# Kernel optimization log

Measured on AMD Instinct MI355X. Metric: run time of the kernel, lower is better.

The kernel has to match this reference:

```python
import jax, jax.numpy as jnp
import numpy as np

N_AE = 64
N_GRAPHS = 4096
N_ELE = 16384
EPS = 1e-5


def _seg_mean(v, idx, num_segments):
    s = jax.ops.segment_sum(v, idx, num_segments=num_segments)
    c = jax.ops.segment_sum(jnp.ones((v.shape[0], 1), v.dtype), idx, num_segments=num_segments)
    return s / jnp.maximum(c, 1.0)


def _batchnorm(h, gamma, beta):
    mu = jnp.mean(h, axis=0)
    var = jnp.mean(jnp.square(h - mu), axis=0)  # biased, as torch BN training fwd
    return (h - mu) * jax.lax.rsqrt(var + EPS) * gamma + beta


def _dist_layer(x, dist_feat, atom_idx, ele_idx, W, b, gamma, beta):
    # x: [N, 2*n_ae]
    pa = jax.nn.relu(_seg_mean(x[:, :N_AE], atom_idx, N_GRAPHS))[atom_idx]   # [N, n_ae]
    pe = jax.nn.relu(_seg_mean(x[:, N_AE:], ele_idx, N_ELE))[ele_idx]        # [N, n_ae]
    h = jnp.concatenate([dist_feat, pa, pe], axis=1)                          # [N, n_de+2*n_ae]
    h = h @ W.T + b                                                           # [N, 2*n_ae]
    h = _batchnorm(h, gamma, beta)
    return jax.nn.relu(h + x)


def setup_inputs() -> dict:
    key = jax.random.key(0)
    ks = jax.random.split(key, 12)
    N = 500000
    n_re = 64
    n_be = 64
    d = 2 * N_AE
    inp = {
        "x": jax.random.normal(ks[0], (N, d), jnp.float32),
        "rdf_feat": jax.random.normal(ks[1], (N, n_re), jnp.float32),
        "bdf_feat": jax.random.normal(ks[2], (N, n_be), jnp.float32),
        "atom_idx": jnp.sort(jax.random.randint(ks[3], (N,), 0, N_GRAPHS)),
        "ele_idx": jax.random.randint(ks[4], (N,), 0, N_ELE),
        "rdf_W": jax.random.normal(ks[5], (d, n_re + d), jnp.float32) * 0.05,
        "rdf_b": jnp.zeros((d,), jnp.float32),
        "rdf_gamma": jnp.ones((d,), jnp.float32),
        "rdf_beta": jnp.zeros((d,), jnp.float32),
        "bdf_W": jax.random.normal(ks[6], (d, n_be + d), jnp.float32) * 0.05,
        "bdf_b": jnp.zeros((d,), jnp.float32),
        "bdf_gamma": jnp.ones((d,), jnp.float32),
        "bdf_beta": jnp.zeros((d,), jnp.float32),
        "fc_W": jax.random.normal(ks[7], (d, 2 * d), jnp.float32) * 0.05,
        "fc_b": jnp.zeros((d,), jnp.float32),
    }
    return inp


def reference(x, rdf_feat, bdf_feat, atom_idx, ele_idx,
              rdf_W, rdf_b, rdf_gamma, rdf_beta,
              bdf_W, bdf_b, bdf_gamma, bdf_beta,
              fc_W, fc_b):
    x1 = _dist_layer(x, rdf_feat, atom_idx, ele_idx, rdf_W, rdf_b, rdf_gamma, rdf_beta)
    x2 = _dist_layer(x, bdf_feat, atom_idx, ele_idx, bdf_W, bdf_b, bdf_gamma, bdf_beta)
    h = jnp.concatenate([x1, x2], axis=1)  # [N, 4*n_ae]
    return jax.nn.relu(h @ fc_W.T + fc_b)  # [N, 2*n_ae]
```

## Files before the change

kernel.cpp:

```cpp
#include <hip/hip_runtime.h>
#include <hip/hip_bf16.h>

#define N_GRAPHS 4096
#define N_ELE 16384
#define EPS 1e-5f

#define A_TAB_OFF 0
#define A_CNT_OFF 262144
#define E_TAB_OFF 266240
#define E_CNT_OFF 1314816
#define STAT_OFF  1331200
#define ZPAD_OFF  1347584
#define ZERO_WORDS 1347588
#define A_TABH_OFF 1347600
#define E_TABH_OFF 1478672
#define W1PK_OFF  2002960
#define FCPK_OFF  2027536
#define SCALE_OFF 2043920
#define SHIFT_OFF 2044176
#define WS_WORDS  2044432

typedef __attribute__((ext_vector_type(8))) short bf16x8;
typedef __attribute__((ext_vector_type(4))) float f32x4;

__device__ __forceinline__ float bf2f(unsigned s) { return __uint_as_float(s << 16); }
__device__ __forceinline__ unsigned f2bf(float f) {
  unsigned u = __float_as_uint(f);
  return (u + 0x7fffu + ((u >> 16) & 1u)) >> 16;
}
__device__ __forceinline__ unsigned pkbf(float a, float b) {
  union { __hip_bfloat16 h; unsigned short u; } ca, cb;
  ca.h = __float2bfloat16(a); cb.h = __float2bfloat16(b);
  return (unsigned)ca.u | ((unsigned)cb.u << 16);
}
__device__ __forceinline__ void gload16(const void* g, void* l) {
  __builtin_amdgcn_global_load_lds(
      (const __attribute__((address_space(1))) unsigned*)g,
      (__attribute__((address_space(3))) unsigned*)l, 16, 0, 0);
}


__global__ void k_prep(const float* __restrict__ W1, const float* __restrict__ W2,
                       const float* __restrict__ fcW, float* __restrict__ ws) {
  int tid = blockIdx.x * 512 + threadIdx.x;
  if (tid < 49152) {
    unsigned short* wpk = (unsigned short*)(ws + W1PK_OFF);
    int L = tid / 24576, rem = tid % 24576;
    int ct = rem / 3072, rem2 = rem % 3072;
    int i = rem2 >> 9, lane = (rem2 >> 3) & 63, j = rem2 & 7;
    int zkb = L ? (i + 2) : (i < 2 ? i : i + 2);
    int zk = zkb * 32 + ((lane >> 4) << 3) + j;
    int kp = L ? (zk - 64) : (zk < 64 ? zk : zk - 64);
    int col = ct * 16 + (lane & 15);
    const float* W = L ? W2 : W1;
    wpk[tid] = (unsigned short)f2bf(W[col * 192 + kp]);
  } else {
    int idx = tid - 49152;
    unsigned short* fpk = (unsigned short*)(ws + FCPK_OFF);
    int ct = idx >> 12, kb = (idx >> 9) & 7, lane = (idx >> 3) & 63, j = idx & 7;
    fpk[idx] = (unsigned short)f2bf(fcW[(ct * 16 + (lane & 15)) * 256 + kb * 32 + ((lane >> 4) << 3) + j]);
  }
}

__global__ void k_seg(const float* __restrict__ x, const int* __restrict__ aidx,
                      const int* __restrict__ eidx, float* __restrict__ ws, int N) {
  float* A_tab = ws + A_TAB_OFF; float* A_cnt = ws + A_CNT_OFF;
  float* E_tab = ws + E_TAB_OFF; float* E_cnt = ws + E_CNT_OFF;
  int t = threadIdx.x;
  int c = t & 63, p = (t >> 6) & 1, s = t >> 7;
  int r0 = blockIdx.x * 256;
  int rend = min(r0 + 256, N);
  if (p == 0) {
    float acc = 0.f, cnt = 0.f; int cur = -1;
    for (int r = r0 + s; r < rend; r += 2) {
      int a = aidx[r];
      float v = x[(size_t)r * 128 + c];
      if (a != cur) {
        if (cur >= 0) { atomicAdd(&A_tab[cur * 64 + c], acc); if (c == 0) atomicAdd(&A_cnt[cur], cnt); }
        cur = a; acc = v; cnt = 1.f;
      } else { acc += v; cnt += 1.f; }
    }
    if (cur >= 0) { atomicAdd(&A_tab[cur * 64 + c], acc); if (c == 0) atomicAdd(&A_cnt[cur], cnt); }
  } else {
    for (int r = r0 + s; r < rend; r += 2) {
      int e = eidx[r];
      float v = x[(size_t)r * 128 + 64 + c];
      atomicAdd(&E_tab[e * 64 + c], v);
      if (c == 0) atomicAdd(&E_cnt[e], 1.f);
    }
  }
}

__global__ void k_fin(float* __restrict__ ws) {
  int i = blockIdx.x * 256 + threadIdx.x;
  unsigned* w32 = (unsigned*)ws;
  if (i < 131072) {
    int e = 2 * i;
    float cnt = fmaxf(ws[A_CNT_OFF + (e >> 6)], 1.f);
    float v0 = fmaxf(ws[A_TAB_OFF + e] / cnt, 0.f);
    float v1 = fmaxf(ws[A_TAB_OFF + e + 1] / cnt, 0.f);
    w32[A_TABH_OFF + i] = f2bf(v0) | (f2bf(v1) << 16);
  }
  if (i < 524288) {
    int e = 2 * i;
    float cnt = fmaxf(ws[E_CNT_OFF + (e >> 6)], 1.f);
    float v0 = fmaxf(ws[E_TAB_OFF + e] / cnt, 0.f);
    float v1 = fmaxf(ws[E_TAB_OFF + e + 1] / cnt, 0.f);
    w32[E_TABH_OFF + i] = f2bf(v0) | (f2bf(v1) << 16);
  }
}

__global__ __launch_bounds__(512) void k_gemm(
    const float* __restrict__ rdf, const float* __restrict__ bdf,
    const int* __restrict__ aidx, const int* __restrict__ eidx,
    float* __restrict__ ws, unsigned* __restrict__ outp, int N) {
  __shared__ __align__(16) char smem[32768];
  const unsigned short* Atabh = (const unsigned short*)(ws + A_TABH_OFF);
  const unsigned short* Etabh = (const unsigned short*)(ws + E_TABH_OFF);
  const void* zpad = (const void*)(ws + ZPAD_OFF);
  int t = threadIdx.x;
  int l = t & 63, w = t >> 6;
  int row0 = blockIdx.x * 64;

  #pragma unroll
  for (int ii = 0; ii < 2; ++ii) {
    int rb = (w * 2 + ii) * 4;
    int r = rb + (l >> 4);
    int srow = row0 + r;
    bool ok = srow < N;
    int s = l & 15;
    int c = (s & 8) | ((s ^ r) & 7);
    const void* src;
    if (c < 8) {
      int ia = ok ? aidx[srow] : 0;
      src = (const void*)(Atabh + ((size_t)ia * 64 + c * 8));
    } else {
      int ie = ok ? eidx[srow] : 0;
      src = (const void*)(Etabh + ((size_t)ie * 64 + (c - 8) * 8));
    }
    if (!ok) src = zpad;
    gload16(src, smem + 16384 + rb * 256);
  }

  {
    int r = t >> 3, c0 = (t & 7) * 2;
    int row = row0 + r;
    bool ok = row < N;
    #pragma unroll
    for (int cc = 0; cc < 2; ++cc) {
      int c = c0 + cc;
      uint4 wv;
      if (ok) {
        const float4* src = (const float4*)(c < 8 ? rdf + (size_t)row * 64 + c * 8
                                                  : bdf + (size_t)row * 64 + (c - 8) * 8);
        float4 f0 = src[0], f1 = src[1];
        wv.x = pkbf(f0.x, f0.y); wv.y = pkbf(f0.z, f0.w);
        wv.z = pkbf(f1.x, f1.y); wv.w = pkbf(f1.z, f1.w);
      } else wv = (uint4){0u, 0u, 0u, 0u};
      int slot = (c & 8) | ((c ^ r) & 7);
      *(uint4*)(smem + r * 256 + slot * 16) = wv;
    }
  }
  __syncthreads();

  int L = w >> 2, ctp = w & 3;
  const unsigned short* WpkL = (const unsigned short*)(ws + W1PK_OFF) + L * 24576;
  f32x4 acc[4][2];
  #pragma unroll
  for (int mt = 0; mt < 4; ++mt)
    #pragma unroll
    for (int cti = 0; cti < 2; ++cti) acc[mt][cti] = (f32x4){0.f, 0.f, 0.f, 0.f};
  int half = l >> 4;
  #pragma unroll
  for (int i = 0; i < 6; ++i) {
    int zkb = L ? (i + 2) : (i < 2 ? i : i + 2);
    int cg = zkb * 4 + half;
    const char* base = smem + (zkb < 4 ? 0 : 16384);
    int cl = cg & 15;
    bf16x8 af[4];
    #pragma unroll
    for (int mt = 0; mt < 4; ++mt) {
      int rr = mt * 16 + (l & 15);
      int slot = (cl & 8) | ((cl ^ rr) & 7);
      af[mt] = *(const bf16x8*)(base + rr * 256 + slot * 16);
    }
    #pragma unroll
    for (int cti = 0; cti < 2; ++cti) {
      bf16x8 bfr = *(const bf16x8*)(WpkL + (((ctp * 2 + cti) * 6 + i) * 64 + l) * 8);
      #pragma unroll
      for (int mt = 0; mt < 4; ++mt)
        acc[mt][cti] = __builtin_amdgcn_mfma_f32_16x16x32_bf16(af[mt], bfr, acc[mt][cti], 0, 0, 0);
    }
  }

  float* stat = ws + STAT_OFF + (blockIdx.x & 31) * 512;
  #pragma unroll
  for (int cti = 0; cti < 2; ++cti) {
    float s = 0.f, q = 0.f;
    #pragma unroll
    for (int mt = 0; mt < 4; ++mt)
      #pragma unroll
      for (int rr = 0; rr < 4; ++rr) { float v = acc[mt][cti][rr]; s += v; q += v * v; }
    s += __shfl_xor(s, 16); s += __shfl_xor(s, 32);
    q += __shfl_xor(q, 16); q += __shfl_xor(q, 32);
    if (l < 16) {
      int gc = L * 128 + ctp * 32 + cti * 16 + l;
      atomicAdd(&stat[gc], s);
      atomicAdd(&stat[256 + gc], q);
    }
  }
  __syncthreads();

  #pragma unroll
  for (int mt = 0; mt < 4; ++mt)
    #pragma unroll
    for (int cti = 0; cti < 2; ++cti)
      #pragma unroll
      for (int rr = 0; rr < 4; ++rr) {
        unsigned ub = pkbf(acc[mt][cti][rr], 0.f) & 0xffffu;
        unsigned pb = (unsigned)__shfl_xor((int)ub, 1);
        if (!(l & 1)) {
          int orow = mt * 16 + ((l >> 4) << 2) + rr;
          int colp = (L * 128 + ctp * 32 + cti * 16 + (l & 15)) >> 1;
          int c = colp >> 2;
          int ec = ((c ^ orow) & 7) | (c & 24);
          *(unsigned*)(smem + orow * 512 + ec * 16 + (colp & 3) * 4) = ub | (pb << 16);
        }
      }
  __syncthreads();
  #pragma unroll
  for (int p = 0; p < 4; ++p) {
    int e = p * 512 + t; int rr = e >> 5, v4 = e & 31;
    int ec = ((v4 ^ rr) & 7) | (v4 & 24);
    uint4 val = *(const uint4*)(smem + rr * 512 + ec * 16);
    if (row0 + rr < N) ((uint4*)outp)[(size_t)(row0 + rr) * 32 + v4] = val;
  }
}

__global__ void k_bnfin(const float* __restrict__ g1, const float* __restrict__ b1,
                        const float* __restrict__ g2, const float* __restrict__ b2,
                        float* __restrict__ ws, int N) {
  int c = threadIdx.x;
  float s = 0.f, q = 0.f;
  for (int m = 0; m < 32; ++m) { s += ws[STAT_OFF + m * 512 + c]; q += ws[STAT_OFF + m * 512 + 256 + c]; }
  float inv = 1.f / (float)N;
  float mu = s * inv;
  float var = fmaxf(q * inv - mu * mu, 0.f);
  int lyr = c >> 7, cc = c & 127;
  float ga = lyr ? g2[cc] : g1[cc];
  float be = lyr ? b2[cc] : b1[cc];
  float sc = ga * rsqrtf(var + EPS);
  ws[SCALE_OFF + c] = sc;
  ws[SHIFT_OFF + c] = be - mu * sc;
}

__global__ __launch_bounds__(512) void k_fc(
    const float* __restrict__ x, const float* __restrict__ fcb,
    float* __restrict__ ws, float* __restrict__ out, int N) {
  __shared__ __align__(16) char smem[32768];
  __shared__ float scsh[512];
  int t = threadIdx.x;
  int l = t & 63, w = t >> 6;
  int r = t >> 3, g = t & 7;
  const unsigned* hp = (const unsigned*)out;
  int row0 = blockIdx.x * 64;
  int row = row0 + r;
  bool ok = row < N;
  uint4 hv[4]; float4 xv[8];
  if (ok) {
    const uint4* hs = (const uint4*)(hp + (size_t)row * 128 + g * 16);
    #pragma unroll
    for (int i = 0; i < 4; ++i) hv[i] = hs[i];
    const float4* xs = (const float4*)(x + (size_t)row * 128 + (g & 3) * 32);
    #pragma unroll
    for (int i = 0; i < 8; ++i) xv[i] = xs[i];
  } else {
    #pragma unroll
    for (int i = 0; i < 4; ++i) hv[i] = (uint4){0u, 0u, 0u, 0u};
    #pragma unroll
    for (int i = 0; i < 8; ++i) xv[i] = (float4){0.f, 0.f, 0.f, 0.f};
  }
  scsh[t] = ws[SCALE_OFF + t];
  __syncthreads();
  {
    unsigned wv[16];
    const unsigned* hu = (const unsigned*)hv;
    const float* xf = (const float*)xv;
    #pragma unroll
    for (int j = 0; j < 16; ++j) {
      int c = g * 32 + 2 * j;
      float lo = bf2f(hu[j] & 0xffffu) * scsh[c]     + scsh[256 + c]     + xf[2 * j];
      float hi = bf2f(hu[j] >> 16)     * scsh[c + 1] + scsh[256 + c + 1] + xf[2 * j + 1];
      wv[j] = pkbf(fmaxf(lo, 0.f), fmaxf(hi, 0.f));
    }
    #pragma unroll
    for (int i = 0; i < 4; ++i) {
      int slot = ((g ^ r ^ i) & 7) | (i << 3);
      *(uint4*)(smem + r * 512 + slot * 16) = ((uint4*)wv)[i];
    }
  }
  __syncthreads();
  f32x4 acc[4];
  #pragma unroll
  for (int mt = 0; mt < 4; ++mt) acc[mt] = (f32x4){0.f, 0.f, 0.f, 0.f};
  const unsigned short* Fpk = (const unsigned short*)(ws + FCPK_OFF);
  int half = l >> 4;
  #pragma unroll
  for (int kb = 0; kb < 8; ++kb) {
    bf16x8 bfr = *(const bf16x8*)(Fpk + ((w * 8 + kb) * 64 + l) * 8);
    #pragma unroll
    for (int mt = 0; mt < 4; ++mt) {
      int rr = mt * 16 + (l & 15);
      int slot = ((kb ^ rr ^ half) & 7) | (half << 3);
      bf16x8 af = *(const bf16x8*)(smem + rr * 512 + slot * 16);
      acc[mt] = __builtin_amdgcn_mfma_f32_16x16x32_bf16(af, bfr, acc[mt], 0, 0, 0);
    }
  }
  float bias = fcb[(w << 4) + (l & 15)];
  __syncthreads();
  #pragma unroll
  for (int mt = 0; mt < 4; ++mt)
    #pragma unroll
    for (int rr = 0; rr < 4; ++rr) {
      int orow = mt * 16 + ((l >> 4) << 2) + rr;
      int col = (w << 4) + (l & 15);
      int c = col >> 2;
      int ec = ((c ^ orow) & 7) | (c & 24);
      *(float*)(smem + orow * 512 + ec * 16 + (col & 3) * 4) = fmaxf(acc[mt][rr] + bias, 0.f);
    }
  __syncthreads();
  #pragma unroll
  for (int p = 0; p < 4; ++p) {
    int e = p * 512 + t; int rr = e >> 5, v4 = e & 31;
    int ec = ((v4 ^ rr) & 7) | (v4 & 24);
    float4 val = *(const float4*)(smem + rr * 512 + ec * 16);
    if (row0 + rr < N) ((float4*)out)[(size_t)(row0 + rr) * 32 + v4] = val;
  }
}

extern "C" void kernel_launch(void* const* d_in, const int* in_sizes, int n_in,
                              void* d_out, int out_size, void* d_ws, size_t ws_size,
                              hipStream_t stream) {
  const float* x    = (const float*)d_in[0];
  const float* rdf  = (const float*)d_in[1];
  const float* bdf  = (const float*)d_in[2];
  const int*   aidx = (const int*)d_in[3];
  const int*   eidx = (const int*)d_in[4];
  const float* rdfW = (const float*)d_in[5];
  const float* rdfG = (const float*)d_in[7];
  const float* rdfBe= (const float*)d_in[8];
  const float* bdfW = (const float*)d_in[9];
  const float* bdfG = (const float*)d_in[11];
  const float* bdfBe= (const float*)d_in[12];
  const float* fcW  = (const float*)d_in[13];
  const float* fcB  = (const float*)d_in[14];
  float* out = (float*)d_out;
  float* ws  = (float*)d_ws;
  int N = in_sizes[0] / 128;
  int nT = (N + 63) / 64;

  hipMemsetAsync(d_ws, 0, (size_t)ZERO_WORDS * 4, stream);
  k_prep<<<160, 512, 0, stream>>>(rdfW, bdfW, fcW, ws);
  k_seg<<<(N + 255) / 256, 256, 0, stream>>>(x, aidx, eidx, ws, N);
  k_fin<<<2048, 256, 0, stream>>>(ws);
  k_gemm<<<nT, 512, 0, stream>>>(rdf, bdf, aidx, eidx, ws, (unsigned*)d_out, N);
  k_bnfin<<<1, 256, 0, stream>>>(rdfG, rdfBe, bdfG, bdfBe, ws, N);
  k_fc<<<nT, 512, 0, stream>>>(x, fcB, ws, out, N);
}
```

Before: 482.9 us.

## Halve block size in gemm and fc kernels so each wave computes more output tiles

Both the distance-layer GEMM and the final FC kernel now use 256 threads per 64-row tile instead of 512. Each wave covers twice as many column tiles, so every A fragment loaded from LDS feeds more MFMAs, and per-thread gather and load work doubles. The gather indices are loaded up front, and s_setprio is raised around the MFMA loops. This trades lower thread-level parallelism and higher register pressure for better operand reuse and fewer waves per tile.

```diff
diff --git a/kernel.cpp b/kernel.cpp
--- a/kernel.cpp
+++ b/kernel.cpp
@@ -38,7 +38,6 @@
       (const __attribute__((address_space(1))) unsigned*)g,
       (__attribute__((address_space(3))) unsigned*)l, 16, 0, 0);
 }
-
 
 __global__ void k_prep(const float* __restrict__ W1, const float* __restrict__ W2,
                        const float* __restrict__ fcW, float* __restrict__ ws) {
@@ -110,7 +109,7 @@
   }
 }
 
-__global__ __launch_bounds__(512) void k_gemm(
+__global__ __launch_bounds__(256) void k_gemm(
     const float* __restrict__ rdf, const float* __restrict__ bdf,
     const int* __restrict__ aidx, const int* __restrict__ eidx,
     float* __restrict__ ws, unsigned* __restrict__ outp, int N) {
@@ -122,32 +121,33 @@
   int l = t & 63, w = t >> 6;
   int row0 = blockIdx.x * 64;
 
-  #pragma unroll
-  for (int ii = 0; ii < 2; ++ii) {
-    int rb = (w * 2 + ii) * 4;
+  int ia4[4], ie4[4];
+  #pragma unroll
+  for (int ii = 0; ii < 4; ++ii) {
+    int srow = row0 + (w * 4 + ii) * 4 + (l >> 4);
+    bool okr = srow < N;
+    int rc = okr ? srow : 0;
+    ia4[ii] = okr ? aidx[rc] : -1;
+    ie4[ii] = okr ? eidx[rc] : -1;
+  }
+  #pragma unroll
+  for (int ii = 0; ii < 4; ++ii) {
+    int rb = (w * 4 + ii) * 4;
     int r = rb + (l >> 4);
-    int srow = row0 + r;
-    bool ok = srow < N;
     int s = l & 15;
     int c = (s & 8) | ((s ^ r) & 7);
     const void* src;
-    if (c < 8) {
-      int ia = ok ? aidx[srow] : 0;
-      src = (const void*)(Atabh + ((size_t)ia * 64 + c * 8));
-    } else {
-      int ie = ok ? eidx[srow] : 0;
-      src = (const void*)(Etabh + ((size_t)ie * 64 + (c - 8) * 8));
-    }
-    if (!ok) src = zpad;
+    if (c < 8) src = (ia4[ii] >= 0) ? (const void*)(Atabh + ((size_t)ia4[ii] * 64 + c * 8)) : zpad;
+    else       src = (ie4[ii] >= 0) ? (const void*)(Etabh + ((size_t)ie4[ii] * 64 + (c - 8) * 8)) : zpad;
     gload16(src, smem + 16384 + rb * 256);
   }
 
   {
-    int r = t >> 3, c0 = (t & 7) * 2;
+    int r = t >> 2, c0 = (t & 3) * 4;
     int row = row0 + r;
     bool ok = row < N;
     #pragma unroll
-    for (int cc = 0; cc < 2; ++cc) {
+    for (int cc = 0; cc < 4; ++cc) {
       int c = c0 + cc;
       uint4 wv;
       if (ok) {
@@ -163,14 +163,15 @@
   }
   __syncthreads();
 
-  int L = w >> 2, ctp = w & 3;
+  int L = w >> 1, cq = w & 1;
   const unsigned short* WpkL = (const unsigned short*)(ws + W1PK_OFF) + L * 24576;
-  f32x4 acc[4][2];
+  f32x4 acc[4][4];
   #pragma unroll
   for (int mt = 0; mt < 4; ++mt)
     #pragma unroll
-    for (int cti = 0; cti < 2; ++cti) acc[mt][cti] = (f32x4){0.f, 0.f, 0.f, 0.f};
+    for (int cti = 0; cti < 4; ++cti) acc[mt][cti] = (f32x4){0.f, 0.f, 0.f, 0.f};
   int half = l >> 4;
+  __builtin_amdgcn_s_setprio(1);
   #pragma unroll
   for (int i = 0; i < 6; ++i) {
     int zkb = L ? (i + 2) : (i < 2 ? i : i + 2);
@@ -185,17 +186,19 @@
       af[mt] = *(const bf16x8*)(base + rr * 256 + slot * 16);
     }
     #pragma unroll
-    for (int cti = 0; cti < 2; ++cti) {
-      bf16x8 bfr = *(const bf16x8*)(WpkL + (((ctp * 2 + cti) * 6 + i) * 64 + l) * 8);
+    for (int cti = 0; cti < 4; ++cti) {
+      int ct = cq * 4 + cti;
+      bf16x8 bfr = *(const bf16x8*)(WpkL + ((ct * 6 + i) * 64 + l) * 8);
       #pragma unroll
       for (int mt = 0; mt < 4; ++mt)
         acc[mt][cti] = __builtin_amdgcn_mfma_f32_16x16x32_bf16(af[mt], bfr, acc[mt][cti], 0, 0, 0);
     }
   }
+  __builtin_amdgcn_s_setprio(0);
 
   float* stat = ws + STAT_OFF + (blockIdx.x & 31) * 512;
   #pragma unroll
-  for (int cti = 0; cti < 2; ++cti) {
+  for (int cti = 0; cti < 4; ++cti) {
     float s = 0.f, q = 0.f;
     #pragma unroll
     for (int mt = 0; mt < 4; ++mt)
@@ -204,7 +207,7 @@
     s += __shfl_xor(s, 16); s += __shfl_xor(s, 32);
     q += __shfl_xor(q, 16); q += __shfl_xor(q, 32);
     if (l < 16) {
-      int gc = L * 128 + ctp * 32 + cti * 16 + l;
+      int gc = L * 128 + (cq * 4 + cti) * 16 + l;
       atomicAdd(&stat[gc], s);
       atomicAdd(&stat[256 + gc], q);
     }
@@ -214,25 +217,25 @@
   #pragma unroll
   for (int mt = 0; mt < 4; ++mt)
     #pragma unroll
-    for (int cti = 0; cti < 2; ++cti)
+    for (int cti = 0; cti < 4; ++cti)
       #pragma unroll
       for (int rr = 0; rr < 4; ++rr) {
         unsigned ub = pkbf(acc[mt][cti][rr], 0.f) & 0xffffu;
         unsigned pb = (unsigned)__shfl_xor((int)ub, 1);
         if (!(l & 1)) {
           int orow = mt * 16 + ((l >> 4) << 2) + rr;
-          int colp = (L * 128 + ctp * 32 + cti * 16 + (l & 15)) >> 1;
-          int c = colp >> 2;
-          int ec = ((c ^ orow) & 7) | (c & 24);
-          *(unsigned*)(smem + orow * 512 + ec * 16 + (colp & 3) * 4) = ub | (pb << 16);
+          int colp = (L * 128 + (cq * 4 + cti) * 16 + (l & 15)) >> 1;
+          int ch = colp >> 2;
+          int cs = ((ch ^ orow) & 7) | (ch & 24);
+          *(unsigned*)(smem + orow * 512 + cs * 16 + (colp & 3) * 4) = ub | (pb << 16);
         }
       }
   __syncthreads();
   #pragma unroll
-  for (int p = 0; p < 4; ++p) {
-    int e = p * 512 + t; int rr = e >> 5, v4 = e & 31;
-    int ec = ((v4 ^ rr) & 7) | (v4 & 24);
-    uint4 val = *(const uint4*)(smem + rr * 512 + ec * 16);
+  for (int p = 0; p < 8; ++p) {
+    int e = p * 256 + t; int rr = e >> 5, v4 = e & 31;
+    int cs = ((v4 ^ rr) & 7) | (v4 & 24);
+    uint4 val = *(const uint4*)(smem + rr * 512 + cs * 16);
     if (row0 + rr < N) ((uint4*)outp)[(size_t)(row0 + rr) * 32 + v4] = val;
   }
 }
@@ -254,86 +257,115 @@
   ws[SHIFT_OFF + c] = be - mu * sc;
 }
 
-__global__ __launch_bounds__(512) void k_fc(
+__device__ __forceinline__ void load_fc(const unsigned* __restrict__ hp, const float* __restrict__ x,
+    int row, int g, uint4* hv, float4* xv, int N) {
+  if (row < N) {
+    const uint4* hs = (const uint4*)((const char*)hp + (size_t)row * 512);
+    hv[0] = hs[2 * g]; hv[1] = hs[2 * g + 1]; hv[2] = hs[2 * g + 16]; hv[3] = hs[2 * g + 17];
+    const float4* xs = (const float4*)(x + (size_t)row * 128 + g * 16);
+    xv[0] = xs[0]; xv[1] = xs[1]; xv[2] = xs[2]; xv[3] = xs[3];
+  } else {
+    #pragma unroll
+    for (int i = 0; i < 4; ++i) { hv[i] = (uint4){0u,0u,0u,0u}; xv[i] = (float4){0.f,0.f,0.f,0.f}; }
+  }
+}
+
+__device__ __forceinline__ void proc_fc(const uint4* hv, const float4* xv, const float* scsh,
+    int r, int g, char* z) {
+  const unsigned* hu = (const unsigned*)hv;
+  const float* xf = (const float*)xv;
+  #pragma unroll
+  for (int hh = 0; hh < 2; ++hh) {
+    #pragma unroll
+    for (int d = 0; d < 2; ++d) {
+      uint4 wq;
+      unsigned* wu = (unsigned*)&wq;
+      #pragma unroll
+      for (int jj = 0; jj < 4; ++jj) {
+        int xi = d * 8 + 2 * jj;
+        int k = g * 16 + hh * 128 + d * 8 + 2 * jj;
+        unsigned hraw = hu[hh * 8 + d * 4 + jj];
+        float lo = bf2f(hraw & 0xffffu) * scsh[k]     + scsh[256 + k]     + xf[xi];
+        float hi = bf2f(hraw >> 16)     * scsh[k + 1] + scsh[256 + k + 1] + xf[xi + 1];
+        wu[jj] = pkbf(fmaxf(lo, 0.f), fmaxf(hi, 0.f));
+      }
+      int c = 2 * g + hh * 16 + d;
+      int kb = c >> 2, hf = c & 3;
+      int slot = (hf << 3) | ((kb ^ r ^ hf) & 7);
+      *(uint4*)(z + r * 512 + slot * 16) = wq;
+    }
+  }
+}
+
+__global__ __launch_bounds__(256) void k_fc(
     const float* __restrict__ x, const float* __restrict__ fcb,
     float* __restrict__ ws, float* __restrict__ out, int N) {
   __shared__ __align__(16) char smem[32768];
   __shared__ float scsh[512];
-  int t = threadIdx.x;
-  int l = t & 63, w = t >> 6;
-  int r = t >> 3, g = t & 7;
+  int t = threadIdx.x, l = t & 63, w = t >> 6;
+  int row0 = blockIdx.x * 64;
   const unsigned* hp = (const unsigned*)out;
-  int row0 = blockIdx.x * 64;
-  int row = row0 + r;
-  bool ok = row < N;
-  uint4 hv[4]; float4 xv[8];
-  if (ok) {
-    const uint4* hs = (const uint4*)(hp + (size_t)row * 128 + g * 16);
-    #pragma unroll
-    for (int i = 0; i < 4; ++i) hv[i] = hs[i];
-    const float4* xs = (const float4*)(x + (size_t)row * 128 + (g & 3) * 32);
-    #pragma unroll
-    for (int i = 0; i < 8; ++i) xv[i] = xs[i];
-  } else {
-    #pragma unroll
-    for (int i = 0; i < 4; ++i) hv[i] = (uint4){0u, 0u, 0u, 0u};
-    #pragma unroll
-    for (int i = 0; i < 8; ++i) xv[i] = (float4){0.f, 0.f, 0.f, 0.f};
-  }
   scsh[t] = ws[SCALE_OFF + t];
-  __syncthreads();
-  {
-    unsigned wv[16];
-    const unsigned* hu = (const unsigned*)hv;
-    const float* xf = (const float*)xv;
-    #pragma unroll
-    for (int j = 0; j < 16; ++j) {
-      int c = g * 32 + 2 * j;
-      float lo = bf2f(hu[j] & 0xffffu) * scsh[c]     + scsh[256 + c]     + xf[2 * j];
-      float hi = bf2f(hu[j] >> 16)     * scsh[c + 1] + scsh[256 + c + 1] + xf[2 * j + 1];
-      wv[j] = pkbf(fmaxf(lo, 0.f), fmaxf(hi, 0.f));
-    }
-    #pragma unroll
-    for (int i = 0; i < 4; ++i) {
-      int slot = ((g ^ r ^ i) & 7) | (i << 3);
-      *(uint4*)(smem + r * 512 + slot * 16) = ((uint4*)wv)[i];
-    }
-  }
-  __syncthreads();
-  f32x4 acc[4];
-  #pragma unroll
-  for (int mt = 0; mt < 4; ++mt) acc[mt] = (f32x4){0.f, 0.f, 0.f, 0.f};
+  scsh[t + 256] = ws[SCALE_OFF + t + 256];
+
+  int rg = t >> 3, g = t & 7;
+  uint4 hv[2][4]; float4 xv[2][4];
+  load_fc(hp, x, row0 + rg, g, hv[0], xv[0], N);
+  load_fc(hp, x, row0 + 32 + rg, g, hv[1], xv[1], N);
+  __syncthreads();
+  proc_fc(hv[0], xv[0], scsh, rg, g, smem);
+  proc_fc(hv[1], xv[1], scsh, 32 + rg, g, smem);
+  __syncthreads();
+
+  f32x4 acc[4][2];
+  #pragma unroll
+  for (int mt = 0; mt < 4; ++mt)
+    #pragma unroll
+    for (int cti = 0; cti < 2; ++cti) acc[mt][cti] = (f32x4){0.f, 0.f, 0.f, 0.f};
   const unsigned short* Fpk = (const unsigned short*)(ws + FCPK_OFF);
   int half = l >> 4;
+  __builtin_amdgcn_s_setprio(1);
   #pragma unroll
   for (int kb = 0; kb < 8; ++kb) {
-    bf16x8 bfr = *(const bf16x8*)(Fpk + ((w * 8 + kb) * 64 + l) * 8);
+    bf16x8 af[4];
     #pragma unroll
     for (int mt = 0; mt < 4; ++mt) {
       int rr = mt * 16 + (l & 15);
       int slot = ((kb ^ rr ^ half) & 7) | (half << 3);
-      bf16x8 af = *(const bf16x8*)(smem + rr * 512 + slot * 16);
-      acc[mt] = __builtin_amdgcn_mfma_f32_16x16x32_bf16(af, bfr, acc[mt], 0, 0, 0);
-    }
-  }
-  float bias = fcb[(w << 4) + (l & 15)];
-  __syncthreads();
-  #pragma unroll
-  for (int mt = 0; mt < 4; ++mt)
-    #pragma unroll
-    for (int rr = 0; rr < 4; ++rr) {
-      int orow = mt * 16 + ((l >> 4) << 2) + rr;
-      int col = (w << 4) + (l & 15);
-      int c = col >> 2;
-      int ec = ((c ^ orow) & 7) | (c & 24);
-      *(float*)(smem + orow * 512 + ec * 16 + (col & 3) * 4) = fmaxf(acc[mt][rr] + bias, 0.f);
-    }
-  __syncthreads();
-  #pragma unroll
-  for (int p = 0; p < 4; ++p) {
-    int e = p * 512 + t; int rr = e >> 5, v4 = e & 31;
-    int ec = ((v4 ^ rr) & 7) | (v4 & 24);
-    float4 val = *(const float4*)(smem + rr * 512 + ec * 16);
+      af[mt] = *(const bf16x8*)(smem + rr * 512 + slot * 16);
+    }
+    #pragma unroll
+    for (int cti = 0; cti < 2; ++cti) {
+      int ct = w * 2 + cti;
+      bf16x8 bfr = *(const bf16x8*)(Fpk + ((ct * 8 + kb) * 64 + l) * 8);
+      #pragma unroll
+      for (int mt = 0; mt < 4; ++mt)
+        acc[mt][cti] = __builtin_amdgcn_mfma_f32_16x16x32_bf16(af[mt], bfr, acc[mt][cti], 0, 0, 0);
+    }
+  }
+  __builtin_amdgcn_s_setprio(0);
+  __syncthreads();
+
+  #pragma unroll
+  for (int cti = 0; cti < 2; ++cti) {
+    float bias = fcb[(w * 2 + cti) * 16 + (l & 15)];
+    #pragma unroll
+    for (int mt = 0; mt < 4; ++mt)
+      #pragma unroll
+      for (int rr = 0; rr < 4; ++rr) {
+        int orow = mt * 16 + ((l >> 4) << 2) + rr;
+        int col = (w * 2 + cti) * 16 + (l & 15);
+        int ch = col >> 2;
+        int cs = ((ch ^ orow) & 7) | (ch & 24);
+        *(float*)(smem + orow * 512 + cs * 16 + (col & 3) * 4) = fmaxf(acc[mt][cti][rr] + bias, 0.f);
+      }
+  }
+  __syncthreads();
+  #pragma unroll
+  for (int p = 0; p < 8; ++p) {
+    int e = p * 256 + t; int rr = e >> 5, v4 = e & 31;
+    int cs = ((v4 ^ rr) & 7) | (v4 & 24);
+    float4 val = *(const float4*)(smem + rr * 512 + cs * 16);
     if (row0 + rr < N) ((float4*)out)[(size_t)(row0 + rr) * 32 + v4] = val;
   }
 }
@@ -363,7 +395,7 @@
   k_prep<<<160, 512, 0, stream>>>(rdfW, bdfW, fcW, ws);
   k_seg<<<(N + 255) / 256, 256, 0, stream>>>(x, aidx, eidx, ws, N);
   k_fin<<<2048, 256, 0, stream>>>(ws);
-  k_gemm<<<nT, 512, 0, stream>>>(rdf, bdf, aidx, eidx, ws, (unsigned*)d_out, N);
+  k_gemm<<<nT, 256, 0, stream>>>(rdf, bdf, aidx, eidx, ws, (unsigned*)d_out, N);
   k_bnfin<<<1, 256, 0, stream>>>(rdfG, rdfBe, bdfG, bdfBe, ws, N);
-  k_fc<<<nT, 512, 0, stream>>>(x, fcB, ws, out, N);
-}
+  k_fc<<<nT, 256, 0, stream>>>(x, fcB, ws, out, N);
+}
```

Result: slower. 512.0 us (+6.0%).

## Remap tiles per XCD, preload weight fragments, and reshape fc loads

Applied to the files above, without the earlier changes.

Adds an XCD-aware block-to-tile remap so that consecutive row tiles land on the same XCD in both the gemm and fc kernels, which is meant to improve L2 locality. Weight B fragments are hoisted into registers before the main loops so their loads can overlap the activation gathers. The fc kernel's loading is reorganised so each thread reads only the x elements it needs rather than duplicating them, with a matching LDS slot remap. The register-resident fragments raise VGPR pressure, which may lower occupancy.

```diff
diff --git a/kernel.cpp b/kernel.cpp
--- a/kernel.cpp
+++ b/kernel.cpp
@@ -38,7 +38,12 @@
       (const __attribute__((address_space(1))) unsigned*)g,
       (__attribute__((address_space(3))) unsigned*)l, 16, 0, 0);
 }
-
+__device__ __forceinline__ int xcd_tile(int bid, int nT) {
+  if (nT < 8) return bid;
+  int q = nT >> 3, r8 = nT & 7;
+  int xcd = bid & 7, i = bid >> 3;
+  return (xcd < r8 ? xcd * (q + 1) : r8 * (q + 1) + (xcd - r8) * q) + i;
+}
 
 __global__ void k_prep(const float* __restrict__ W1, const float* __restrict__ W2,
                        const float* __restrict__ fcW, float* __restrict__ ws) {
@@ -113,14 +118,24 @@
 __global__ __launch_bounds__(512) void k_gemm(
     const float* __restrict__ rdf, const float* __restrict__ bdf,
     const int* __restrict__ aidx, const int* __restrict__ eidx,
-    float* __restrict__ ws, unsigned* __restrict__ outp, int N) {
+    float* __restrict__ ws, unsigned* __restrict__ outp, int N, int nT) {
   __shared__ __align__(16) char smem[32768];
   const unsigned short* Atabh = (const unsigned short*)(ws + A_TABH_OFF);
   const unsigned short* Etabh = (const unsigned short*)(ws + E_TABH_OFF);
   const void* zpad = (const void*)(ws + ZPAD_OFF);
   int t = threadIdx.x;
   int l = t & 63, w = t >> 6;
-  int row0 = blockIdx.x * 64;
+  int tile = xcd_tile(blockIdx.x, nT);
+  int row0 = tile * 64;
+  int L = w >> 2, ctp = w & 3;
+  const unsigned short* WpkL = (const unsigned short*)(ws + W1PK_OFF) + L * 24576;
+
+  bf16x8 Bfr[12];
+  #pragma unroll
+  for (int i = 0; i < 6; ++i)
+    #pragma unroll
+    for (int cti = 0; cti < 2; ++cti)
+      Bfr[i * 2 + cti] = *(const bf16x8*)(WpkL + (((ctp * 2 + cti) * 6 + i) * 64 + l) * 8);
 
   #pragma unroll
   for (int ii = 0; ii < 2; ++ii) {
@@ -131,13 +146,8 @@
     int s = l & 15;
     int c = (s & 8) | ((s ^ r) & 7);
     const void* src;
-    if (c < 8) {
-      int ia = ok ? aidx[srow] : 0;
-      src = (const void*)(Atabh + ((size_t)ia * 64 + c * 8));
-    } else {
-      int ie = ok ? eidx[srow] : 0;
-      src = (const void*)(Etabh + ((size_t)ie * 64 + (c - 8) * 8));
-    }
+    if (c < 8) { int ia = ok ? aidx[srow] : 0; src = (const void*)(Atabh + ((size_t)ia * 64 + c * 8)); }
+    else       { int ie = ok ? eidx[srow] : 0; src = (const void*)(Etabh + ((size_t)ie * 64 + (c - 8) * 8)); }
     if (!ok) src = zpad;
     gload16(src, smem + 16384 + rb * 256);
   }
@@ -163,8 +173,6 @@
   }
   __syncthreads();
 
-  int L = w >> 2, ctp = w & 3;
-  const unsigned short* WpkL = (const unsigned short*)(ws + W1PK_OFF) + L * 24576;
   f32x4 acc[4][2];
   #pragma unroll
   for (int mt = 0; mt < 4; ++mt)
@@ -186,10 +194,9 @@
     }
     #pragma unroll
     for (int cti = 0; cti < 2; ++cti) {
-      bf16x8 bfr = *(const bf16x8*)(WpkL + (((ctp * 2 + cti) * 6 + i) * 64 + l) * 8);
       #pragma unroll
       for (int mt = 0; mt < 4; ++mt)
-        acc[mt][cti] = __builtin_amdgcn_mfma_f32_16x16x32_bf16(af[mt], bfr, acc[mt][cti], 0, 0, 0);
+        acc[mt][cti] = __builtin_amdgcn_mfma_f32_16x16x32_bf16(af[mt], Bfr[i * 2 + cti], acc[mt][cti], 0, 0, 0);
     }
   }
 
@@ -204,7 +211,7 @@
     s += __shfl_xor(s, 16); s += __shfl_xor(s, 32);
     q += __shfl_xor(q, 16); q += __shfl_xor(q, 32);
     if (l < 16) {
-      int gc = L * 128 + ctp * 32 + cti * 16 + l;
+      int gc = L * 128 + (ctp * 2 + cti) * 16 + l;
       atomicAdd(&stat[gc], s);
       atomicAdd(&stat[256 + gc], q);
     }
@@ -221,7 +228,7 @@
         unsigned pb = (unsigned)__shfl_xor((int)ub, 1);
         if (!(l & 1)) {
           int orow = mt * 16 + ((l >> 4) << 2) + rr;
-          int colp = (L * 128 + ctp * 32 + cti * 16 + (l & 15)) >> 1;
+          int colp = (L * 128 + (ctp * 2 + cti) * 16 + (l & 15)) >> 1;
           int c = colp >> 2;
           int ec = ((c ^ orow) & 7) | (c & 24);
           *(unsigned*)(smem + orow * 512 + ec * 16 + (colp & 3) * 4) = ub | (pb << 16);
@@ -254,86 +261,103 @@
   ws[SHIFT_OFF + c] = be - mu * sc;
 }
 
+__device__ __forceinline__ void load_fc(const unsigned* __restrict__ hp, const float* __restrict__ x,
+    int row, int g, uint4* hv, float4* xv, int N) {
+  if (row < N) {
+    const uint4* hs = (const uint4*)((const char*)hp + (size_t)row * 512);
+    hv[0] = hs[2 * g]; hv[1] = hs[2 * g + 1]; hv[2] = hs[2 * g + 16]; hv[3] = hs[2 * g + 17];
+    const float4* xs = (const float4*)(x + (size_t)row * 128 + g * 16);
+    xv[0] = xs[0]; xv[1] = xs[1]; xv[2] = xs[2]; xv[3] = xs[3];
+  } else {
+    #pragma unroll
+    for (int i = 0; i < 4; ++i) { hv[i] = (uint4){0u,0u,0u,0u}; xv[i] = (float4){0.f,0.f,0.f,0.f}; }
+  }
+}
+
+__device__ __forceinline__ void proc_fc(const uint4* hv, const float4* xv, const float* scsh,
+    int r, int g, char* z) {
+  const unsigned* hu = (const unsigned*)hv;
+  const float* xf = (const float*)xv;
+  #pragma unroll
+  for (int hh = 0; hh < 2; ++hh) {
+    #pragma unroll
+    for (int d = 0; d < 2; ++d) {
+      uint4 wq;
+      unsigned* wu = (unsigned*)&wq;
+      #pragma unroll
+      for (int jj = 0; jj < 4; ++jj) {
+        int xi = d * 8 + 2 * jj;
+        int k = g * 16 + hh * 128 + d * 8 + 2 * jj;
+        unsigned hraw = hu[hh * 8 + d * 4 + jj];
+        float lo = bf2f(hraw & 0xffffu) * scsh[k]     + scsh[256 + k]     + xf[xi];
+        float hi = bf2f(hraw >> 16)     * scsh[k + 1] + scsh[256 + k + 1] + xf[xi + 1];
+        wu[jj] = pkbf(fmaxf(lo, 0.f), fmaxf(hi, 0.f));
+      }
+      int c = 2 * g + hh * 16 + d;
+      int kb = c >> 2, hf = c & 3;
+      int slot = (hf << 3) | ((kb ^ r ^ hf) & 7);
+      *(uint4*)(z + r * 512 + slot * 16) = wq;
+    }
+  }
+}
+
 __global__ __launch_bounds__(512) void k_fc(
     const float* __restrict__ x, const float* __restrict__ fcb,
-    float* __restrict__ ws, float* __restrict__ out, int N) {
+    float* __restrict__ ws, float* __restrict__ out, int N, int nT) {
   __shared__ __align__(16) char smem[32768];
   __shared__ float scsh[512];
-  int t = threadIdx.x;
-  int l = t & 63, w = t >> 6;
-  int r = t >> 3, g = t & 7;
+  int t = threadIdx.x, l = t & 63, w = t >> 6;
+  int tile = xcd_tile(blockIdx.x, nT);
+  int row0 = tile * 64;
   const unsigned* hp = (const unsigned*)out;
-  int row0 = blockIdx.x * 64;
-  int row = row0 + r;
-  bool ok = row < N;
-  uint4 hv[4]; float4 xv[8];
-  if (ok) {
-    const uint4* hs = (const uint4*)(hp + (size_t)row * 128 + g * 16);
-    #pragma unroll
-    for (int i = 0; i < 4; ++i) hv[i] = hs[i];
-    const float4* xs = (const float4*)(x + (size_t)row * 128 + (g & 3) * 32);
-    #pragma unroll
-    for (int i = 0; i < 8; ++i) xv[i] = xs[i];
-  } else {
-    #pragma unroll
-    for (int i = 0; i < 4; ++i) hv[i] = (uint4){0u, 0u, 0u, 0u};
-    #pragma unroll
-    for (int i = 0; i < 8; ++i) xv[i] = (float4){0.f, 0.f, 0.f, 0.f};
-  }
-  scsh[t] = ws[SCALE_OFF + t];
-  __syncthreads();
-  {
-    unsigned wv[16];
-    const unsigned* hu = (const unsigned*)hv;
-    const float* xf = (const float*)xv;
-    #pragma unroll
-    for (int j = 0; j < 16; ++j) {
-      int c = g * 32 + 2 * j;
-      float lo = bf2f(hu[j] & 0xffffu) * scsh[c]     + scsh[256 + c]     + xf[2 * j];
-      float hi = bf2f(hu[j] >> 16)     * scsh[c + 1] + scsh[256 + c + 1] + xf[2 * j + 1];
-      wv[j] = pkbf(fmaxf(lo, 0.f), fmaxf(hi, 0.f));
-    }
-    #pragma unroll
-    for (int i = 0; i < 4; ++i) {
-      int slot = ((g ^ r ^ i) & 7) | (i << 3);
-      *(uint4*)(smem + r * 512 + slot * 16) = ((uint4*)wv)[i];
-    }
-  }
-  __syncthreads();
-  f32x4 acc[4];
-  #pragma unroll
-  for (int mt = 0; mt < 4; ++mt) acc[mt] = (f32x4){0.f, 0.f, 0.f, 0.f};
   const unsigned short* Fpk = (const unsigned short*)(ws + FCPK_OFF);
   int half = l >> 4;
+
+  bf16x8 Bfr[8];
+  #pragma unroll
+  for (int kb = 0; kb < 8; ++kb)
+    Bfr[kb] = *(const bf16x8*)(Fpk + ((w * 8 + kb) * 64 + l) * 8);
+
+  scsh[t] = ws[SCALE_OFF + t];
+  int rg = t >> 3, g = t & 7;
+  uint4 hv[4]; float4 xv[4];
+  load_fc(hp, x, row0 + rg, g, hv, xv, N);
+  float bias = fcb[(w << 4) + (l & 15)];
+  __syncthreads();
+  proc_fc(hv, xv, scsh, rg, g, smem);
+  __syncthreads();
+
+  f32x4 acc[4];
+  #pragma unroll
+  for (int mt = 0; mt < 4; ++mt) acc[mt] = (f32x4){0.f, 0.f, 0.f, 0.f};
   #pragma unroll
   for (int kb = 0; kb < 8; ++kb) {
-    bf16x8 bfr = *(const bf16x8*)(Fpk + ((w * 8 + kb) * 64 + l) * 8);
     #pragma unroll
     for (int mt = 0; mt < 4; ++mt) {
       int rr = mt * 16 + (l & 15);
       int slot = ((kb ^ rr ^ half) & 7) | (half << 3);
       bf16x8 af = *(const bf16x8*)(smem + rr * 512 + slot * 16);
-      acc[mt] = __builtin_amdgcn_mfma_f32_16x16x32_bf16(af, bfr, acc[mt], 0, 0, 0);
-    }
-  }
-  float bias = fcb[(w << 4) + (l & 15)];
-  __syncthreads();
+      acc[mt] = __builtin_amdgcn_mfma_f32_16x16x32_bf16(af, Bfr[kb], acc[mt], 0, 0, 0);
+    }
+  }
+  __syncthreads();
+
   #pragma unroll
   for (int mt = 0; mt < 4; ++mt)
     #pragma unroll
     for (int rr = 0; rr < 4; ++rr) {
       int orow = mt * 16 + ((l >> 4) << 2) + rr;
       int col = (w << 4) + (l & 15);
-      int c = col >> 2;
-      int ec = ((c ^ orow) & 7) | (c & 24);
-      *(float*)(smem + orow * 512 + ec * 16 + (col & 3) * 4) = fmaxf(acc[mt][rr] + bias, 0.f);
+      int ch = col >> 2;
+      int cs = ((ch ^ orow) & 7) | (ch & 24);
+      *(float*)(smem + orow * 512 + cs * 16 + (col & 3) * 4) = fmaxf(acc[mt][rr] + bias, 0.f);
     }
   __syncthreads();
   #pragma unroll
   for (int p = 0; p < 4; ++p) {
     int e = p * 512 + t; int rr = e >> 5, v4 = e & 31;
-    int ec = ((v4 ^ rr) & 7) | (v4 & 24);
-    float4 val = *(const float4*)(smem + rr * 512 + ec * 16);
+    int cs = ((v4 ^ rr) & 7) | (v4 & 24);
+    float4 val = *(const float4*)(smem + rr * 512 + cs * 16);
     if (row0 + rr < N) ((float4*)out)[(size_t)(row0 + rr) * 32 + v4] = val;
   }
 }
@@ -363,7 +387,7 @@
   k_prep<<<160, 512, 0, stream>>>(rdfW, bdfW, fcW, ws);
   k_seg<<<(N + 255) / 256, 256, 0, stream>>>(x, aidx, eidx, ws, N);
   k_fin<<<2048, 256, 0, stream>>>(ws);
-  k_gemm<<<nT, 512, 0, stream>>>(rdf, bdf, aidx, eidx, ws, (unsigned*)d_out, N);
+  k_gemm<<<nT, 512, 0, stream>>>(rdf, bdf, aidx, eidx, ws, (unsigned*)d_out, N, nT);
   k_bnfin<<<1, 256, 0, stream>>>(rdfG, rdfBe, bdfG, bdfBe, ws, N);
-  k_fc<<<nT, 512, 0, stream>>>(x, fcB, ws, out, N);
-}
+  k_fc<<<nT, 512, 0, stream>>>(x, fcB, ws, out, N, nT);
+}
```

New measurement: 455.0 us. 1.06x faster.
